# Kernel tuning notes

Hardware: AMD Instinct MI355X
Metric: run time of the kernel (lower is better)

## Reference

```python
import jax, jax.numpy as jnp
import numpy as np

B, N, C, H, NL, NH = 8, 1024, 256, 512, 3, 8


def setup_inputs() -> dict:
    key = jax.random.key(0)
    ks = jax.random.split(key, 16)
    g = lambda k, shape: jax.random.normal(k, shape, jnp.float32) * 0.02
    return dict(
        concept_features=jax.random.normal(ks[0], (B, N, C), jnp.float32),
        adjacency_matrix=jax.random.uniform(ks[1], (B, N, N), jnp.float32),
        edge_types=jax.random.randint(ks[2], (B, N, N), 0, 10),
        concept_mask=jnp.ones((B, N), bool),
        W_emb=g(ks[3], (H, C)), b_emb=jnp.zeros((H,), jnp.float32),
        W_in=g(ks[4], (NL, 3 * H, H)), b_in=jnp.zeros((NL, 3 * H), jnp.float32),
        W_out=g(ks[5], (NL, H, H)), b_out=jnp.zeros((NL, H), jnp.float32),
        W_conv=g(ks[6], (NL, H, H)), b_conv=jnp.zeros((NL, H), jnp.float32),
        W_cls=g(ks[7], (1, H)), b_cls=jnp.zeros((1,), jnp.float32),
        W_diff=g(ks[8], (5, H)), b_diff=jnp.zeros((5,), jnp.float32),
        W_pre=g(ks[9], (1, 2 * H)), b_pre=jnp.zeros((1,), jnp.float32),
        W_pool=g(ks[10], (H, H)), b_pool=jnp.zeros((H,), jnp.float32),
    )


def reference(concept_features, adjacency_matrix, edge_types, concept_mask,
              W_emb, b_emb, W_in, b_in, W_out, b_out, W_conv, b_conv,
              W_cls, b_cls, W_diff, b_diff, W_pre, b_pre, W_pool, b_pool):
    Bq, Nc, _ = concept_features.shape
    Hd = W_emb.shape[0]
    dh = Hd // NH

    def mha(x, Wi, bi, Wo, bo):
        # torch nn.MultiheadAttention with batch_first=False: the (B,N,H)
        # input is treated as (seq=B, batch=N, embed=H) -> attention over B.
        qkv = x @ Wi.T + bi                      # (B,N,3H)
        q, k, v = jnp.split(qkv, 3, axis=-1)
        rs = lambda t: t.reshape(Bq, Nc, NH, dh)
        q, k, v = rs(q), rs(k), rs(v)
        sc = jnp.einsum('inhd,jnhd->nhij', q, k) / jnp.sqrt(jnp.float32(dh))
        a = jax.nn.softmax(sc, axis=-1)          # (N,NH,B,B)
        o = jnp.einsum('nhij,jnhd->inhd', a, v).reshape(Bq, Nc, Hd)
        return o @ Wo.T + bo

    def ln(x):  # F.layer_norm, no affine
        m = x.mean(-1, keepdims=True)
        v = ((x - m) ** 2).mean(-1, keepdims=True)
        return (x - m) * jax.lax.rsqrt(v + 1e-5)

    x = concept_features @ W_emb.T + b_emb       # (B,N,H)
    for l in range(W_in.shape[0]):
        att = mha(x, W_in[l], b_in[l], W_out[l], b_out[l])
        conv = att @ W_conv[l].T + b_conv[l]
        agg = jnp.einsum('bij,bjh->bih', adjacency_matrix, conv)
        x = ln(x + agg)

    mastery = x @ W_cls.T + b_cls                # (B,N,1)
    diff = x @ W_diff.T + b_diff                 # (B,N,5)

    # O(N^2) pairwise loop -> bilinear decomposition:
    # score(i,j) = x_i @ W_pre[:, :H].T + x_j @ W_pre[:, H:].T + b
    h1 = (x @ W_pre[:, :Hd].T)[..., 0]           # (B,N)
    h2 = (x @ W_pre[:, Hd:].T)[..., 0]           # (B,N)
    pair = h1[:, :, None] + h2[:, None, :] + b_pre[0]  # (B,N,N)
    off = ~np.eye(Nc, dtype=bool).reshape(-1)    # static mask, i!=j row-major
    prereq = pair.reshape(Bq, Nc * Nc)[:, off][..., None]  # (B,N*(N-1),1)

    graph = x.mean(axis=1) @ W_pool.T + b_pool   # (B,H)
    return (x, mastery, diff, prereq, graph)
```

## Files before the change

kernel.cpp:

```cpp
#include <hip/hip_runtime.h>
#include <hip/hip_bf16.h>

typedef unsigned short ushort_t;
typedef __attribute__((ext_vector_type(4))) float floatx4;
typedef __attribute__((ext_vector_type(8))) __bf16 bf16x8;
typedef __attribute__((ext_vector_type(4))) unsigned short ushortx4;
typedef __attribute__((ext_vector_type(8))) unsigned short ushortx8;

static __device__ __forceinline__ float b2f(ushort_t u) {
  union { unsigned int i; float f; } v; v.i = ((unsigned int)u) << 16; return v.f;
}
static __device__ __forceinline__ ushort_t f2b(float f) {
  unsigned int x = __float_as_uint(f);
  unsigned int r = (x + 0x7fffu + ((x >> 16) & 1u)) >> 16;
  return (ushort_t)r;
}
static __device__ __forceinline__ void glds16(const ushort_t* g, ushort_t* l) {
  __builtin_amdgcn_global_load_lds(
      (const __attribute__((address_space(1))) unsigned int*)g,
      (__attribute__((address_space(3))) unsigned int*)l, 16, 0, 0);
}

template<int MODE>
__global__ __launch_bounds__(512, 2) void gemm8p(
    const ushort_t* __restrict__ Ab, const ushort_t* __restrict__ Bm,
    const float* __restrict__ bias,
    ushort_t* __restrict__ C0, ushort_t* __restrict__ C1,
    int N, int K)
{
  __shared__ __align__(16) ushort_t As[2 * 16384];
  __shared__ __align__(16) ushort_t Bs[2 * 16384];
  const int tid  = threadIdx.x;
  const int wid  = tid >> 6;
  const int lane = tid & 63;
  const int quad = lane >> 4;
  const int l16  = lane & 15;
  const int rx   = l16 & 7;
  const int lin = blockIdx.y * gridDim.x + blockIdx.x;
  const int m0 = (lin % gridDim.y) * 256;
  const int n0 = (lin / gridDim.y) * 256;
  const int NT = K >> 6;

  const int srow = tid >> 3;
  const int scj  = ((tid & 7) ^ (srow & 7)) * 8;
  const long abase = (long)(m0 + srow) * K + scj;
  const long bbase = (long)(n0 + srow) * K + scj;

  floatx4 acc[16][2];
#pragma unroll
  for (int i = 0; i < 16; ++i) {
    acc[i][0] = (floatx4){0.f, 0.f, 0.f, 0.f};
    acc[i][1] = (floatx4){0.f, 0.f, 0.f, 0.f};
  }

#define STG_A(bf, h, t) do { const long k0_ = (long)(t) << 6; \
    glds16(Ab + abase + (long)((h) * 128     ) * K + k0_, &As[(bf) * 16384 + (h) * 8192 + tid * 8]); \
    glds16(Ab + abase + (long)((h) * 128 + 64) * K + k0_, &As[(bf) * 16384 + (h) * 8192 + 4096 + tid * 8]); } while (0)
#define STG_B(bf, h, t) do { const long k0_ = (long)(t) << 6; \
    glds16(Bm + bbase + (long)((h) * 128     ) * K + k0_, &Bs[(bf) * 16384 + (h) * 8192 + tid * 8]); \
    glds16(Bm + bbase + (long)((h) * 128 + 64) * K + k0_, &Bs[(bf) * 16384 + (h) * 8192 + 4096 + tid * 8]); } while (0)

  STG_A(0, 0, 0); STG_B(0, 0, 0); STG_B(0, 1, 0); STG_A(0, 1, 0);

  for (int t = 0; t < NT; ++t) {
    const int c = t & 1;
    const ushort_t* AsC = &As[c * 16384];
    const ushort_t* BsC = &Bs[c * 16384];
    const bool pf = (t + 1 < NT);
    bf16x8 a[8];
    bf16x8 bfr[2][2];

    asm volatile("s_waitcnt vmcnt(2)" ::: "memory");
    __builtin_amdgcn_s_barrier();
#pragma unroll
    for (int j = 0; j < 2; ++j)
#pragma unroll
      for (int kc = 0; kc < 2; ++kc)
        bfr[j][kc] = *(const bf16x8*)(&BsC[(wid * 32 + j * 16 + l16) * 64 +
                                           (((kc * 4 + quad) ^ rx) << 3)]);
#pragma unroll
    for (int f = 0; f < 8; ++f)
      a[f] = *(const bf16x8*)(&AsC[(f * 16 + l16) * 64 + ((quad ^ rx) << 3)]);
    if (pf) STG_A(c ^ 1, 0, t + 1);
    __builtin_amdgcn_s_setprio(1);
#pragma unroll
    for (int f = 0; f < 8; ++f) {
      acc[f][0] = __builtin_amdgcn_mfma_f32_16x16x32_bf16(a[f], bfr[0][0], acc[f][0], 0, 0, 0);
      acc[f][1] = __builtin_amdgcn_mfma_f32_16x16x32_bf16(a[f], bfr[1][0], acc[f][1], 0, 0, 0);
    }
    __builtin_amdgcn_s_setprio(0);

#pragma unroll
    for (int f = 0; f < 8; ++f)
      a[f] = *(const bf16x8*)(&AsC[(f * 16 + l16) * 64 + (((4 + quad) ^ rx) << 3)]);
    if (pf) STG_B(c ^ 1, 0, t + 1);
    __builtin_amdgcn_s_setprio(1);
#pragma unroll
    for (int f = 0; f < 8; ++f) {
      acc[f][0] = __builtin_amdgcn_mfma_f32_16x16x32_bf16(a[f], bfr[0][1], acc[f][0], 0, 0, 0);
      acc[f][1] = __builtin_amdgcn_mfma_f32_16x16x32_bf16(a[f], bfr[1][1], acc[f][1], 0, 0, 0);
    }
    __builtin_amdgcn_s_setprio(0);

    if (pf) { asm volatile("s_waitcnt vmcnt(4)" ::: "memory"); }
    else    { asm volatile("s_waitcnt vmcnt(0)" ::: "memory"); }
    __builtin_amdgcn_s_barrier();
#pragma unroll
    for (int f = 0; f < 8; ++f)
      a[f] = *(const bf16x8*)(&AsC[(128 + f * 16 + l16) * 64 + ((quad ^ rx) << 3)]);
    if (pf) STG_B(c ^ 1, 1, t + 1);
    __builtin_amdgcn_s_setprio(1);
#pragma unroll
    for (int f = 0; f < 8; ++f) {
      acc[8 + f][0] = __builtin_amdgcn_mfma_f32_16x16x32_bf16(a[f], bfr[0][0], acc[8 + f][0], 0, 0, 0);
      acc[8 + f][1] = __builtin_amdgcn_mfma_f32_16x16x32_bf16(a[f], bfr[1][0], acc[8 + f][1], 0, 0, 0);
    }
    __builtin_amdgcn_s_setprio(0);

#pragma unroll
    for (int f = 0; f < 8; ++f)
      a[f] = *(const bf16x8*)(&AsC[(128 + f * 16 + l16) * 64 + (((4 + quad) ^ rx) << 3)]);
    if (pf) STG_A(c ^ 1, 1, t + 1);
    __builtin_amdgcn_s_setprio(1);
#pragma unroll
    for (int f = 0; f < 8; ++f) {
      acc[8 + f][0] = __builtin_amdgcn_mfma_f32_16x16x32_bf16(a[f], bfr[0][1], acc[8 + f][0], 0, 0, 0);
      acc[8 + f][1] = __builtin_amdgcn_mfma_f32_16x16x32_bf16(a[f], bfr[1][1], acc[8 + f][1], 0, 0, 0);
    }
    __builtin_amdgcn_s_setprio(0);
  }
#undef STG_A
#undef STG_B

#pragma unroll
  for (int fj = 0; fj < 2; ++fj) {
    int col = n0 + wid * 32 + fj * 16 + l16;
    float bv = (bias != nullptr) ? bias[col] : 0.f;
#pragma unroll
    for (int fi = 0; fi < 16; ++fi) {
      int mbase = m0 + fi * 16 + quad * 4;
      if constexpr (MODE == 1) {
#pragma unroll
        for (int r = 0; r < 4; ++r)
          C0[(long)(mbase + r) * N + col] = f2b(acc[fi][fj][r] + bv);
      } else {
        ushort_t* o = (n0 < 512) ? C0 : C1;
        const int cw = (n0 < 512) ? 512 : 1536;
        const int cc = (n0 < 512) ? col : col - 512;
#pragma unroll
        for (int r = 0; r < 4; ++r)
          o[(long)(mbase + r) * cw + cc] = f2b(acc[fi][fj][r] + bv);
      }
    }
  }
}

template<int MODE>
static __device__ __forceinline__ void gemm_core(
    const ushort_t* __restrict__ Ab, const ushort_t* __restrict__ Bm,
    const float* __restrict__ bias,
    ushort_t* __restrict__ outB, ushort_t* __restrict__ C1,
    int N, int K, int m0, int n0, int kbeg, int kend,
    ushort_t* As, ushort_t* Bs)
{
  const int tid  = threadIdx.x;
  const int wid  = tid >> 6;
  const int lane = tid & 63;
  const int quad = lane >> 4;
  const int l16  = lane & 15;

  const int wr = (wid >> 1) * 64;
  const int wc = (wid & 1) * 64;

  const int srow = tid >> 3;
  const int scj  = ((tid & 7) ^ (srow & 7)) * 8;
  const long abase = (long)(m0 + srow) * K + scj;
  const long bbase = (long)(n0 + srow) * K + scj;

  floatx4 acc[4][4];
#pragma unroll
  for (int i = 0; i < 4; ++i)
#pragma unroll
    for (int j = 0; j < 4; ++j) acc[i][j] = (floatx4){0.f, 0.f, 0.f, 0.f};

  const int rx = l16 & 7;

  for (int k0 = kbeg; k0 < kend; k0 += 64) {
    __syncthreads();
#pragma unroll
    for (int p = 0; p < 4; ++p)
      glds16(Ab + abase + 32 * p * (long)K + k0, &As[tid * 8 + p * 2048]);
#pragma unroll
    for (int p = 0; p < 4; ++p)
      glds16(Bm + bbase + 32 * p * (long)K + k0, &Bs[tid * 8 + p * 2048]);
    __syncthreads();

#pragma unroll
    for (int kk = 0; kk < 2; ++kk) {
      bf16x8 a[4], b[4];
#pragma unroll
      for (int i = 0; i < 4; ++i)
        a[i] = *(const bf16x8*)(&As[(wr + i * 16 + l16) * 64 +
                                    (((kk * 4 + quad) ^ rx) << 3)]);
#pragma unroll
      for (int j = 0; j < 4; ++j)
        b[j] = *(const bf16x8*)(&Bs[(wc + j * 16 + l16) * 64 +
                                    (((kk * 4 + quad) ^ rx) << 3)]);
#pragma unroll
      for (int i = 0; i < 4; ++i)
#pragma unroll
        for (int j = 0; j < 4; ++j)
          acc[i][j] = __builtin_amdgcn_mfma_f32_16x16x32_bf16(a[i], b[j], acc[i][j], 0, 0, 0);
    }
  }

#pragma unroll
  for (int j = 0; j < 4; ++j) {
    int col = n0 + wc + j * 16 + l16;
    float bv = (bias != nullptr) ? bias[col] : 0.f;
#pragma unroll
    for (int i = 0; i < 4; ++i) {
      int mbase = m0 + wr + i * 16 + quad * 4;
      if constexpr (MODE == 1) {
#pragma unroll
        for (int r = 0; r < 4; ++r)
          outB[(long)(mbase + r) * N + col] = f2b(acc[i][j][r] + bv);
      } else {
        int b = mbase >> 10, jrow = mbase & 1023;
        ushortx4 pk;
#pragma unroll
        for (int r = 0; r < 4; ++r) pk[r] = f2b(acc[i][j][r] + bv);
        *(ushortx4*)(outB + ((long)b * N + col) * 1024 + jrow) = pk;
      }
    }
  }
}

template<int MODE, int KS>
__global__ __launch_bounds__(256, 3) void gemm_bt(
    const ushort_t* __restrict__ Ab, const ushort_t* __restrict__ Bm,
    const float* __restrict__ bias,
    ushort_t* __restrict__ C0, ushort_t* __restrict__ C1,
    int N, int K, long aBatch, long bBatch, long cBatch)
{
  __shared__ __align__(16) ushort_t As[128 * 64];
  __shared__ __align__(16) ushort_t Bs[128 * 64];
  const int lin = blockIdx.y * gridDim.x + blockIdx.x;
  const int m0 = (lin % gridDim.y) * 128;
  const int n0 = (lin / gridDim.y) * 128;
  const int z  = (KS > 1) ? (int)(blockIdx.z / KS) : blockIdx.z;
  const int kq = (KS > 1) ? (int)(blockIdx.z % KS) : 0;
  const int kbeg = kq * (K / KS);
  const int kend = kbeg + (K / KS);
  ushort_t* outB = (KS >= 2 && kq == 1) ? C1 : C0;
  gemm_core<MODE>(Ab + (long)z * aBatch, Bm + (long)z * bBatch, bias,
                  outB + ((MODE == 1) ? (long)z * cBatch : 0), C1,
                  N, K, m0, n0, kbeg, kend, As, Bs);
}

__global__ __launch_bounds__(256, 3) void setup_gemm(
    const ushort_t* __restrict__ Wcb, const ushort_t* __restrict__ WoT,
    ushort_t* __restrict__ Wfb,
    const ushort_t* __restrict__ Winb, const ushort_t* __restrict__ WembT,
    ushort_t* __restrict__ Wq0t)
{
  __shared__ __align__(16) ushort_t As[128 * 64];
  __shared__ __align__(16) ushort_t Bs[128 * 64];
  const int lin = blockIdx.x;
  const int z = blockIdx.z;
  if (z < 3) {
    if (lin >= 16) return;
    const long off = (long)z * 262144;
    gemm_core<1>(Wcb + off, WoT + off, nullptr, Wfb + off, nullptr,
                 512, 512, (lin & 3) * 128, (lin >> 2) * 128, 0, 512, As, Bs);
  } else {
    gemm_core<1>(Winb, WembT, nullptr, Wq0t, nullptr,
                 256, 512, (lin % 12) * 128, (lin / 12) * 128, 0, 512, As, Bs);
  }
}

__global__ __launch_bounds__(256) void prep_kernel(
    const float* __restrict__ Win,  ushort_t* __restrict__ Winb,
    const float* __restrict__ Wemb, ushort_t* __restrict__ Wq0,
    const float* __restrict__ Wconv, ushort_t* __restrict__ Wcb,
    const float* __restrict__ ADJ,  ushort_t* __restrict__ ADJb,
    const float* __restrict__ CF,   ushort_t* __restrict__ CFb,
    const float* __restrict__ Wout, ushort_t* __restrict__ WoT,
    const float* __restrict__ bout, const float* __restrict__ bconv,
    float* __restrict__ bfused,
    ushort_t* __restrict__ WembT,
    const float* __restrict__ bemb, const float* __restrict__ bin0,
    float* __restrict__ bcat,
    const float* __restrict__ Wpool, float* __restrict__ WpT)
{
  __shared__ float tile[64][65];
  const int bid = blockIdx.x, tid = threadIdx.x;
  if (bid < 6720) {
    const float* src; ushort_t* dst; long i;
    if (bid < 1152)      { src = Win;   dst = Winb; i = (long)bid * 256 + tid; }
    else if (bid < 1216) { src = Wemb;  dst = Wq0;  i = (long)(bid - 1152) * 256 + tid; }
    else if (bid < 1600) { src = Wconv; dst = Wcb;  i = (long)(bid - 1216) * 256 + tid; }
    else if (bid < 5696) { src = ADJ;   dst = ADJb; i = (long)(bid - 1600) * 256 + tid; }
    else                 { src = CF;    dst = CFb;  i = (long)(bid - 5696) * 256 + tid; }
    floatx4 a = ((const floatx4*)src)[2 * i];
    floatx4 b = ((const floatx4*)src)[2 * i + 1];
    ushortx4 ha, hb;
#pragma unroll
    for (int r = 0; r < 4; ++r) { ha[r] = f2b(a[r]); hb[r] = f2b(b[r]); }
    ((ushortx4*)dst)[2 * i] = ha; ((ushortx4*)dst)[2 * i + 1] = hb;
  } else if (bid < 6912) {
    const int t = bid - 6720;
    const int z = t >> 6, k0 = ((t >> 3) & 7) * 64, j0 = (t & 7) * 64;
    const long base = (long)z * 262144;
#pragma unroll
    for (int p = 0; p < 16; ++p) {
      int idx = tid + p * 256;
      int jj = idx >> 6, kk = idx & 63;
      tile[jj][kk] = Wout[base + (long)(j0 + jj) * 512 + k0 + kk];
    }
    __syncthreads();
#pragma unroll
    for (int p = 0; p < 16; ++p) {
      int idx = tid + p * 256;
      int kk = idx >> 6, jj = idx & 63;
      WoT[base + (long)(k0 + kk) * 512 + j0 + jj] = f2b(tile[jj][kk]);
    }
  } else if (bid < 6944) {
    const int t = bid - 6912;
    const int j0 = (t >> 2) * 64, k0 = (t & 3) * 64;
#pragma unroll
    for (int p = 0; p < 16; ++p) {
      int idx = tid + p * 256;
      int jj = idx >> 6, kk = idx & 63;
      tile[jj][kk] = Wemb[(long)(j0 + jj) * 256 + k0 + kk];
    }
    __syncthreads();
#pragma unroll
    for (int p = 0; p < 16; ++p) {
      int idx = tid + p * 256;
      int kk = idx >> 6, jj = idx & 63;
      WembT[(long)(k0 + kk) * 512 + j0 + jj] = f2b(tile[jj][kk]);
    }
  } else if (bid < 7328) {
    const int w = tid >> 6, lane = tid & 63;
    const int gi = (bid - 6944) * 4 + w;
    const int l = gi >> 9, o = gi & 511;
    float p = 0.f;
#pragma unroll
    for (int k = 0; k < 8; ++k)
      p += Wconv[(long)l * 262144 + (long)o * 512 + lane + 64 * k] *
           bout[l * 512 + lane + 64 * k];
#pragma unroll
    for (int msk = 1; msk <= 32; msk <<= 1) p += __shfl_xor(p, msk);
    if (lane == 0) bfused[gi] = p + bconv[l * 512 + o];
  } else if (bid < 7712) {
    const int w = tid >> 6, lane = tid & 63;
    const int o = (bid - 7328) * 4 + w;
    float p = 0.f;
#pragma unroll
    for (int k = 0; k < 8; ++k)
      p += Win[(long)o * 512 + lane + 64 * k] * bemb[lane + 64 * k];
#pragma unroll
    for (int msk = 1; msk <= 32; msk <<= 1) p += __shfl_xor(p, msk);
    if (lane == 0) bcat[512 + o] = p + bin0[o];
  } else if (bid < 7714) {
    int idx = (bid - 7712) * 256 + tid;
    bcat[idx] = bemb[idx];
  } else {
    const int t = bid - 7714;
    const int j0 = (t >> 3) * 64, k0 = (t & 7) * 64;
#pragma unroll
    for (int p = 0; p < 16; ++p) {
      int idx = tid + p * 256;
      int jj = idx >> 6, kk = idx & 63;
      tile[jj][kk] = Wpool[(long)(j0 + jj) * 512 + k0 + kk];
    }
    __syncthreads();
#pragma unroll
    for (int p = 0; p < 16; ++p) {
      int idx = tid + p * 256;
      int kk = idx >> 6, jj = idx & 63;
      WpT[(long)(k0 + kk) * 512 + j0 + jj] = tile[jj][kk];
    }
  }
}

__global__ __launch_bounds__(512, 8) void attn_kernel(
    const ushort_t* __restrict__ qkv, ushort_t* __restrict__ outp)
{
  __shared__ ushort_t qs[8 * 1544];
  __shared__ float aw[8][64];
  const int tid = threadIdx.x;
  const int n = blockIdx.x;

  const ushort_t* src = qkv + (long)n * 1536;
#pragma unroll
  for (int p = 0; p < 3; ++p) {
    int c = tid + p * 512;
    int i = c / 192, off = (c % 192) * 8;
    *(ushortx8*)(&qs[i * 1544 + off]) =
        *(const ushortx8*)(src + (long)i * 1024 * 1536 + off);
  }
  __syncthreads();

  const int h    = tid >> 6;
  const int lane = tid & 63;
  const int i = lane >> 3, j = lane & 7;
  const ushort_t* qrow = &qs[i * 1544 + h * 64];
  const ushort_t* krow = &qs[j * 1544 + 512 + h * 64];
  float s = 0.f;
#pragma unroll
  for (int c8 = 0; c8 < 8; ++c8) {
    ushortx8 qa = *(const ushortx8*)(qrow + c8 * 8);
    ushortx8 ka = *(const ushortx8*)(krow + c8 * 8);
#pragma unroll
    for (int r = 0; r < 8; ++r) s += b2f(qa[r]) * b2f(ka[r]);
  }
  s *= 0.125f;

  float m = s;
  m = fmaxf(m, __shfl_xor(m, 1));
  m = fmaxf(m, __shfl_xor(m, 2));
  m = fmaxf(m, __shfl_xor(m, 4));
  float e = __expf(s - m);
  float sum = e;
  sum += __shfl_xor(sum, 1);
  sum += __shfl_xor(sum, 2);
  sum += __shfl_xor(sum, 4);
  aw[h][lane] = e / sum;

  float vv[8];
#pragma unroll
  for (int jj = 0; jj < 8; ++jj)
    vv[jj] = b2f(qs[jj * 1544 + 1024 + h * 64 + lane]);
  const long ob = (long)n * 512 + h * 64 + lane;
#pragma unroll
  for (int ii = 0; ii < 8; ++ii) {
    float acc = 0.f;
#pragma unroll
    for (int jj = 0; jj < 8; ++jj) acc += aw[h][ii * 8 + jj] * vv[jj];
    outp[ob + (long)ii * 1024 * 512] = f2b(acc);
  }
}

__global__ __launch_bounds__(256) void ln_kernel(
    const ushort_t* __restrict__ xb,
    const ushort_t* __restrict__ aggA, const ushort_t* __restrict__ aggB,
    ushort_t* __restrict__ outB)
{
  const int w = threadIdx.x >> 6, lane = threadIdx.x & 63;
  const long base = ((long)blockIdx.x * 4 + w) * 512;
  float v[8];
  float s = 0.f;
#pragma unroll
  for (int k = 0; k < 8; ++k) {
    long idx = base + lane + 64 * k;
    v[k] = b2f(xb[idx]) + b2f(aggA[idx]) + b2f(aggB[idx]);
    s += v[k];
  }
#pragma unroll
  for (int msk = 1; msk <= 32; msk <<= 1) s += __shfl_xor(s, msk);
  float mean = s * (1.f / 512.f);
  float vv = 0.f;
#pragma unroll
  for (int k = 0; k < 8; ++k) { float d = v[k] - mean; vv += d * d; }
#pragma unroll
  for (int msk = 1; msk <= 32; msk <<= 1) vv += __shfl_xor(vv, msk);
  float inv = rsqrtf(vv * (1.f / 512.f) + 1e-5f);
#pragma unroll
  for (int k = 0; k < 8; ++k)
    outB[base + lane + 64 * k] = f2b((v[k] - mean) * inv);
}

__global__ __launch_bounds__(256) void final_ln_heads_kernel(
    const ushort_t* __restrict__ xb,
    const ushort_t* __restrict__ aggA, const ushort_t* __restrict__ aggB,
    float* __restrict__ out_x,
    const float* __restrict__ Wcls, const float* __restrict__ bcls,
    const float* __restrict__ Wdiff, const float* __restrict__ bdiff,
    const float* __restrict__ Wpre,
    float* __restrict__ mastery, float* __restrict__ diff,
    float* __restrict__ h1, float* __restrict__ h2,
    float* __restrict__ xp)
{
  __shared__ float sp4[4][512];
  const int w = threadIdx.x >> 6, lane = threadIdx.x & 63;
  const long row = (long)blockIdx.x * 4 + w;
  const long base = row * 512;
  float v[8];
  float s = 0.f;
#pragma unroll
  for (int k = 0; k < 8; ++k) {
    long idx = base + lane + 64 * k;
    v[k] = b2f(xb[idx]) + b2f(aggA[idx]) + b2f(aggB[idx]);
    s += v[k];
  }
#pragma unroll
  for (int msk = 1; msk <= 32; msk <<= 1) s += __shfl_xor(s, msk);
  float mean = s * (1.f / 512.f);
  float vv = 0.f;
#pragma unroll
  for (int k = 0; k < 8; ++k) { float d = v[k] - mean; vv += d * d; }
#pragma unroll
  for (int msk = 1; msk <= 32; msk <<= 1) vv += __shfl_xor(vv, msk);
  float inv = rsqrtf(vv * (1.f / 512.f) + 1e-5f);
#pragma unroll
  for (int k = 0; k < 8; ++k) {
    v[k] = (v[k] - mean) * inv;
    out_x[base + lane + 64 * k] = v[k];
    sp4[w][lane + 64 * k] = v[k];
  }
  __syncthreads();
  for (int t = threadIdx.x; t < 512; t += 256)
    xp[(long)blockIdx.x * 512 + t] =
        sp4[0][t] + sp4[1][t] + sp4[2][t] + sp4[3][t];
#pragma unroll
  for (int o = 0; o < 8; ++o) {
    const float* wp = (o == 0) ? Wcls
                    : (o <= 5) ? (Wdiff + (o - 1) * 512)
                    : (o == 6) ? Wpre : (Wpre + 512);
    float p = 0.f;
#pragma unroll
    for (int k = 0; k < 8; ++k) p += v[k] * wp[lane + 64 * k];
#pragma unroll
    for (int msk = 1; msk <= 32; msk <<= 1) p += __shfl_xor(p, msk);
    if (lane == 0) {
      if (o == 0)      mastery[row] = p + bcls[0];
      else if (o <= 5) diff[row * 5 + (o - 1)] = p + bdiff[o - 1];
      else if (o == 6) h1[row] = p;
      else             h2[row] = p;
    }
  }
}

__global__ __launch_bounds__(256) void epi_kernel(
    const float* __restrict__ h1, const float* __restrict__ h2,
    const float* __restrict__ bpre, float* __restrict__ outp,
    const float* __restrict__ xp, float* __restrict__ xq)
{
  const int bid = blockIdx.x;
  if (bid < 8184) {
    const int g = bid * 256 + threadIdx.x;
    const int t = g * 4;
    const int b = t / 1047552;
    const int r = t - b * 1047552;
    const float bp = bpre[0];
    const float* h1b = h1 + b * 1024;
    const float* h2b = h2 + b * 1024;
    floatx4 o;
#pragma unroll
    for (int k = 0; k < 4; ++k) {
      int rk = r + k;
      int i = rk / 1023;
      int pos = rk - i * 1023;
      int j = pos + (pos >= i);
      o[k] = h1b[i] + bp + h2b[j];
    }
    *(floatx4*)(outp + t) = o;
  } else {
    const int q0 = bid - 8184;
    const float* p = xp + (long)q0 * 32 * 512;
#pragma unroll
    for (int cc = 0; cc < 2; ++cc) {
      int c = threadIdx.x + cc * 256;
      float s = 0.f;
#pragma unroll
      for (int q = 0; q < 32; ++q) s += p[q * 512 + c];
      xq[(long)q0 * 512 + c] = s;
    }
  }
}

__global__ __launch_bounds__(256) void graph_kernel(
    const float* __restrict__ xq, const float* __restrict__ WpT,
    const float* __restrict__ bpool, float* __restrict__ g)
{
  __shared__ float xms[512];
  const int b = blockIdx.x;
  const float* xb = xq + (long)b * 8 * 512;
#pragma unroll
  for (int cc = 0; cc < 2; ++cc) {
    int c = threadIdx.x + cc * 256;
    float s = 0.f;
#pragma unroll
    for (int p = 0; p < 8; ++p) s += xb[p * 512 + c];
    xms[c] = s;
  }
  __syncthreads();
#pragma unroll
  for (int oo = 0; oo < 2; ++oo) {
    int o = threadIdx.x + oo * 256;
    float acc = 0.f;
    for (int h = 0; h < 512; ++h) acc += xms[h] * WpT[h * 512 + o];
    g[b * 512 + o] = acc * (1.f / 1024.f) + bpool[o];
  }
}

extern "C" void kernel_launch(void* const* d_in, const int* in_sizes, int n_in,
                              void* d_out, int out_size, void* d_ws, size_t ws_size,
                              hipStream_t stream)
{
  const float* CF    = (const float*)d_in[0];
  const float* ADJ   = (const float*)d_in[1];
  const float* Wemb  = (const float*)d_in[4];
  const float* bemb  = (const float*)d_in[5];
  const float* Win   = (const float*)d_in[6];
  const float* bin   = (const float*)d_in[7];
  const float* Wout  = (const float*)d_in[8];
  const float* bout  = (const float*)d_in[9];
  const float* Wconv = (const float*)d_in[10];
  const float* bconv = (const float*)d_in[11];
  const float* Wcls  = (const float*)d_in[12];
  const float* bcls  = (const float*)d_in[13];
  const float* Wdiff = (const float*)d_in[14];
  const float* bdiff = (const float*)d_in[15];
  const float* Wpre  = (const float*)d_in[16];
  const float* bpre  = (const float*)d_in[17];
  const float* Wpool = (const float*)d_in[18];
  const float* bpool = (const float*)d_in[19];

  ushort_t* W = (ushort_t*)d_ws;
  ushort_t* xb   = W;
  ushort_t* qkvb = W + 4194304;
  ushort_t* cT    = qkvb;
  ushort_t* aggA  = qkvb + 4194304;
  ushort_t* aggB  = qkvb + 8388608;
  ushort_t* WoT   = qkvb + 4194304;
  ushort_t* Wcb   = qkvb + 4980736;
  ushort_t* WembT = qkvb + 5767168;
  ushort_t* Winb = W + 16777216;
  ushort_t* Wfb  = W + 19136512;
  ushort_t* ADJb = W + 19922944;
  ushort_t* CFb  = W + 28311552;
  ushort_t* Wq0  = W + 32505856;
  float* bfused = (float*)(W + 33030144);
  float* bcat   = bfused + 1536;
  float* h1     = bcat + 2048;
  float* h2     = h1 + 8192;
  float* xp     = h2 + 8192;
  float* xq     = xp + 1048576;
  float* WpT    = xq + 32768;

  float* out_x       = (float*)d_out;
  float* out_mastery = out_x + 4194304;
  float* out_diff    = out_mastery + 8192;
  float* out_prereq  = out_diff + 40960;
  float* out_graph   = out_prereq + 8380416;
  ushort_t* aob = (ushort_t*)out_x;

  dim3 blk(256);
  dim3 blk8(512);

  prep_kernel<<<dim3(7778), blk, 0, stream>>>(
      Win, Winb, Wemb, Wq0, Wconv, Wcb, ADJ, ADJb, CF, CFb,
      Wout, WoT, bout, bconv, bfused, WembT, bemb, bin, bcat,
      Wpool, WpT);
  setup_gemm<<<dim3(24, 1, 4), blk, 0, stream>>>(
      Wcb, WoT, Wfb, Winb, WembT, Wq0 + 512 * 256);

  for (int l = 0; l < 3; ++l) {
    if (l == 0) {
      gemm8p<3><<<dim3(8, 32), blk8, 0, stream>>>(
          CFb, Wq0, bcat, xb, qkvb, 2048, 256);
    } else {
      gemm8p<1><<<dim3(6, 32), blk8, 0, stream>>>(
          xb, Winb + (long)l * 786432, bin + l * 1536,
          qkvb, nullptr, 1536, 512);
    }
    attn_kernel<<<dim3(1024), dim3(512), 0, stream>>>(qkvb, aob);
    gemm_bt<2, 1><<<dim3(4, 64, 1), blk, 0, stream>>>(
        aob, Wfb + (long)l * 262144, bfused + l * 512,
        cT, nullptr, 512, 512, 0, 0, 0);
    gemm_bt<1, 2><<<dim3(4, 8, 16), blk, 0, stream>>>(
        ADJb, cT, nullptr, aggA, aggB,
        512, 1024, 1048576, 524288, 524288);
    if (l < 2)
      ln_kernel<<<dim3(2048), blk, 0, stream>>>(xb, aggA, aggB, xb);
    else
      final_ln_heads_kernel<<<dim3(2048), blk, 0, stream>>>(
          xb, aggA, aggB, out_x, Wcls, bcls, Wdiff, bdiff, Wpre,
          out_mastery, out_diff, h1, h2, xp);
  }

  epi_kernel<<<dim3(8248), blk, 0, stream>>>(h1, h2, bpre, out_prereq,
                                             xp, xq);
  graph_kernel<<<dim3(8), blk, 0, stream>>>(xq, WpT, bpool, out_graph);
}
```

Measured before the change: 420.8 us.

## Fuse attention with fused out-proj/conv GEMM into one kernel per layer

Merges the per-column attention kernel and the following 512x512 projection GEMM into one kernel. Each block handles 4 sequence columns (32 rows), keeps the attention output in LDS, runs MFMA against the fused weight read directly from global memory, and writes the transposed cT layout. This removes one launch and the global round trip of the attention output. In exchange each block streams the whole 512x512 weight from global/L2 without LDS staging, the grid drops to 256 blocks, and the large LDS footprint limits occupancy.

```diff
diff --git a/kernel.cpp b/kernel.cpp
--- a/kernel.cpp
+++ b/kernel.cpp
@@ -159,7 +159,7 @@
 static __device__ __forceinline__ void gemm_core(
     const ushort_t* __restrict__ Ab, const ushort_t* __restrict__ Bm,
     const float* __restrict__ bias,
-    ushort_t* __restrict__ outB, ushort_t* __restrict__ C1,
+    ushort_t* __restrict__ outB,
     int N, int K, int m0, int n0, int kbeg, int kend,
     ushort_t* As, ushort_t* Bs)
 {
@@ -221,17 +221,9 @@
 #pragma unroll
     for (int i = 0; i < 4; ++i) {
       int mbase = m0 + wr + i * 16 + quad * 4;
-      if constexpr (MODE == 1) {
-#pragma unroll
-        for (int r = 0; r < 4; ++r)
-          outB[(long)(mbase + r) * N + col] = f2b(acc[i][j][r] + bv);
-      } else {
-        int b = mbase >> 10, jrow = mbase & 1023;
-        ushortx4 pk;
-#pragma unroll
-        for (int r = 0; r < 4; ++r) pk[r] = f2b(acc[i][j][r] + bv);
-        *(ushortx4*)(outB + ((long)b * N + col) * 1024 + jrow) = pk;
-      }
+#pragma unroll
+      for (int r = 0; r < 4; ++r)
+        outB[(long)(mbase + r) * N + col] = f2b(acc[i][j][r] + bv);
     }
   }
 }
@@ -254,7 +246,7 @@
   const int kend = kbeg + (K / KS);
   ushort_t* outB = (KS >= 2 && kq == 1) ? C1 : C0;
   gemm_core<MODE>(Ab + (long)z * aBatch, Bm + (long)z * bBatch, bias,
-                  outB + ((MODE == 1) ? (long)z * cBatch : 0), C1,
+                  outB + ((MODE == 1) ? (long)z * cBatch : 0),
                   N, K, m0, n0, kbeg, kend, As, Bs);
 }
 
@@ -271,10 +263,10 @@
   if (z < 3) {
     if (lin >= 16) return;
     const long off = (long)z * 262144;
-    gemm_core<1>(Wcb + off, WoT + off, nullptr, Wfb + off, nullptr,
+    gemm_core<1>(Wcb + off, WoT + off, nullptr, Wfb + off,
                  512, 512, (lin & 3) * 128, (lin >> 2) * 128, 0, 512, As, Bs);
   } else {
-    gemm_core<1>(Winb, WembT, nullptr, Wq0t, nullptr,
+    gemm_core<1>(Winb, WembT, nullptr, Wq0t,
                  256, 512, (lin % 12) * 128, (lin / 12) * 128, 0, 512, As, Bs);
   }
 }
@@ -385,61 +377,108 @@
   }
 }
 
-__global__ __launch_bounds__(512, 8) void attn_kernel(
-    const ushort_t* __restrict__ qkv, ushort_t* __restrict__ outp)
-{
-  __shared__ ushort_t qs[8 * 1544];
-  __shared__ float aw[8][64];
+__global__ __launch_bounds__(512) void attn_conv_kernel(
+    const ushort_t* __restrict__ qkv, const ushort_t* __restrict__ Wf,
+    const float* __restrict__ bfused, ushort_t* __restrict__ cT)
+{
+  __shared__ ushort_t qs[32 * 1544];
+  __shared__ float aw[4][8][64];
+  __shared__ __align__(16) ushort_t ao[32 * 520];
   const int tid = threadIdx.x;
-  const int n = blockIdx.x;
-
-  const ushort_t* src = qkv + (long)n * 1536;
-#pragma unroll
-  for (int p = 0; p < 3; ++p) {
+  const int n0 = blockIdx.x * 4;
+
+#pragma unroll
+  for (int p = 0; p < 12; ++p) {
     int c = tid + p * 512;
-    int i = c / 192, off = (c % 192) * 8;
-    *(ushortx8*)(&qs[i * 1544 + off]) =
-        *(const ushortx8*)(src + (long)i * 1024 * 1536 + off);
+    int rr = c / 192, off = (c % 192) * 8;
+    int dn = rr >> 3, i = rr & 7;
+    *(ushortx8*)(&qs[rr * 1544 + off]) =
+        *(const ushortx8*)(qkv + ((long)(i * 1024 + n0 + dn) * 1536 + off));
   }
   __syncthreads();
 
   const int h    = tid >> 6;
   const int lane = tid & 63;
   const int i = lane >> 3, j = lane & 7;
-  const ushort_t* qrow = &qs[i * 1544 + h * 64];
-  const ushort_t* krow = &qs[j * 1544 + 512 + h * 64];
-  float s = 0.f;
-#pragma unroll
-  for (int c8 = 0; c8 < 8; ++c8) {
-    ushortx8 qa = *(const ushortx8*)(qrow + c8 * 8);
-    ushortx8 ka = *(const ushortx8*)(krow + c8 * 8);
-#pragma unroll
-    for (int r = 0; r < 8; ++r) s += b2f(qa[r]) * b2f(ka[r]);
-  }
-  s *= 0.125f;
-
-  float m = s;
-  m = fmaxf(m, __shfl_xor(m, 1));
-  m = fmaxf(m, __shfl_xor(m, 2));
-  m = fmaxf(m, __shfl_xor(m, 4));
-  float e = __expf(s - m);
-  float sum = e;
-  sum += __shfl_xor(sum, 1);
-  sum += __shfl_xor(sum, 2);
-  sum += __shfl_xor(sum, 4);
-  aw[h][lane] = e / sum;
-
-  float vv[8];
-#pragma unroll
-  for (int jj = 0; jj < 8; ++jj)
-    vv[jj] = b2f(qs[jj * 1544 + 1024 + h * 64 + lane]);
-  const long ob = (long)n * 512 + h * 64 + lane;
-#pragma unroll
-  for (int ii = 0; ii < 8; ++ii) {
-    float acc = 0.f;
-#pragma unroll
-    for (int jj = 0; jj < 8; ++jj) acc += aw[h][ii * 8 + jj] * vv[jj];
-    outp[ob + (long)ii * 1024 * 512] = f2b(acc);
+
+#pragma unroll
+  for (int dn = 0; dn < 4; ++dn) {
+    const ushort_t* qrow = &qs[(dn * 8 + i) * 1544 + h * 64];
+    const ushort_t* krow = &qs[(dn * 8 + j) * 1544 + 512 + h * 64];
+    float s = 0.f;
+#pragma unroll
+    for (int c8 = 0; c8 < 8; ++c8) {
+      ushortx8 qa = *(const ushortx8*)(qrow + c8 * 8);
+      ushortx8 ka = *(const ushortx8*)(krow + c8 * 8);
+#pragma unroll
+      for (int r = 0; r < 8; ++r) s += b2f(qa[r]) * b2f(ka[r]);
+    }
+    s *= 0.125f;
+    float m = s;
+    m = fmaxf(m, __shfl_xor(m, 1));
+    m = fmaxf(m, __shfl_xor(m, 2));
+    m = fmaxf(m, __shfl_xor(m, 4));
+    float e = __expf(s - m);
+    float sum = e;
+    sum += __shfl_xor(sum, 1);
+    sum += __shfl_xor(sum, 2);
+    sum += __shfl_xor(sum, 4);
+    aw[dn][h][lane] = e / sum;
+  }
+
+#pragma unroll
+  for (int dn = 0; dn < 4; ++dn) {
+    float vv[8];
+#pragma unroll
+    for (int jj = 0; jj < 8; ++jj)
+      vv[jj] = b2f(qs[(dn * 8 + jj) * 1544 + 1024 + h * 64 + lane]);
+#pragma unroll
+    for (int ii = 0; ii < 8; ++ii) {
+      float acc = 0.f;
+#pragma unroll
+      for (int jj = 0; jj < 8; ++jj) acc += aw[dn][h][ii * 8 + jj] * vv[jj];
+      ao[(ii * 4 + dn) * 520 + h * 64 + lane] = f2b(acc);
+    }
+  }
+  __syncthreads();
+
+  const int quad = lane >> 4, l16 = lane & 15;
+  const int cb = h * 64;
+  floatx4 acc[2][4];
+#pragma unroll
+  for (int mf = 0; mf < 2; ++mf)
+#pragma unroll
+    for (int nf = 0; nf < 4; ++nf) acc[mf][nf] = (floatx4){0.f, 0.f, 0.f, 0.f};
+
+  for (int ks = 0; ks < 16; ++ks) {
+    const int c0 = ks * 32 + quad * 8;
+    bf16x8 bfr[4], afr[2];
+#pragma unroll
+    for (int nf = 0; nf < 4; ++nf)
+      bfr[nf] = *(const bf16x8*)(Wf + (long)(cb + nf * 16 + l16) * 512 + c0);
+#pragma unroll
+    for (int mf = 0; mf < 2; ++mf)
+      afr[mf] = *(const bf16x8*)(&ao[(mf * 16 + l16) * 520 + c0]);
+#pragma unroll
+    for (int mf = 0; mf < 2; ++mf)
+#pragma unroll
+      for (int nf = 0; nf < 4; ++nf)
+        acc[mf][nf] = __builtin_amdgcn_mfma_f32_16x16x32_bf16(
+            afr[mf], bfr[nf], acc[mf][nf], 0, 0, 0);
+  }
+
+#pragma unroll
+  for (int nf = 0; nf < 4; ++nf) {
+    int col = cb + nf * 16 + l16;
+    float bv = bfused[col];
+#pragma unroll
+    for (int mf = 0; mf < 2; ++mf) {
+      int b = mf * 4 + quad;
+      ushortx4 pk;
+#pragma unroll
+      for (int r = 0; r < 4; ++r) pk[r] = f2b(acc[mf][nf][r] + bv);
+      *(ushortx4*)(cT + ((long)(b * 512 + col)) * 1024 + n0) = pk;
+    }
   }
 }
 
@@ -622,7 +661,6 @@
   ushort_t* W = (ushort_t*)d_ws;
   ushort_t* xb   = W;
   ushort_t* qkvb = W + 4194304;
-  ushort_t* cT    = qkvb;
   ushort_t* aggA  = qkvb + 4194304;
   ushort_t* aggB  = qkvb + 8388608;
   ushort_t* WoT   = qkvb + 4194304;
@@ -646,7 +684,7 @@
   float* out_diff    = out_mastery + 8192;
   float* out_prereq  = out_diff + 40960;
   float* out_graph   = out_prereq + 8380416;
-  ushort_t* aob = (ushort_t*)out_x;
+  ushort_t* cT = (ushort_t*)out_x;
 
   dim3 blk(256);
   dim3 blk8(512);
@@ -667,10 +705,8 @@
           xb, Winb + (long)l * 786432, bin + l * 1536,
           qkvb, nullptr, 1536, 512);
     }
-    attn_kernel<<<dim3(1024), dim3(512), 0, stream>>>(qkvb, aob);
-    gemm_bt<2, 1><<<dim3(4, 64, 1), blk, 0, stream>>>(
-        aob, Wfb + (long)l * 262144, bfused + l * 512,
-        cT, nullptr, 512, 512, 0, 0, 0);
+    attn_conv_kernel<<<dim3(256), dim3(512), 0, stream>>>(
+        qkvb, Wfb + (long)l * 262144, bfused + l * 512, cT);
     gemm_bt<1, 2><<<dim3(4, 8, 16), blk, 0, stream>>>(
         ADJb, cT, nullptr, aggA, aggB,
         512, 1024, 1048576, 524288, 524288);
```

Result: slower. 468.5 us (+11.3%).
